# Optimization experiments

Measured on AMD Instinct MI355X. Metric: run time of the kernel, lower is better.

## Reference

```python
import jax, jax.numpy as jnp
import numpy as np

NUM_GROUPS = 32
EPS = 1e-6


def setup_inputs() -> dict:
    key = jax.random.key(0)
    ks = jax.random.split(key, 8)
    B, C, H, W = 2, 512, 64, 64
    s = 1.0 / np.sqrt(C)
    return {
        "x": jax.random.normal(ks[0], (B, C, H, W), dtype=jnp.float32),
        "norm_w": jnp.ones((C,), jnp.float32),
        "norm_b": jnp.zeros((C,), jnp.float32),
        "wq": jax.random.normal(ks[1], (C, C), dtype=jnp.float32) * s,
        "bq": jnp.zeros((C,), jnp.float32),
        "wk": jax.random.normal(ks[2], (C, C), dtype=jnp.float32) * s,
        "bk": jnp.zeros((C,), jnp.float32),
        "wv": jax.random.normal(ks[3], (C, C), dtype=jnp.float32) * s,
        "bv": jnp.zeros((C,), jnp.float32),
        "wp": jax.random.normal(ks[4], (C, C), dtype=jnp.float32) * s,
        "bp": jnp.zeros((C,), jnp.float32),
    }


def _group_norm(x, w, b):
    # x: [B, C, H, W], 32 groups, eps=1e-6, affine
    B, C, H, W = x.shape
    g = x.reshape(B, NUM_GROUPS, C // NUM_GROUPS, H, W)
    mu = jnp.mean(g, axis=(2, 3, 4), keepdims=True)
    var = jnp.mean(jnp.square(g - mu), axis=(2, 3, 4), keepdims=True)
    g = (g - mu) * jax.lax.rsqrt(var + EPS)
    x = g.reshape(B, C, H, W)
    return x * w[None, :, None, None] + b[None, :, None, None]


def _conv1x1(x, w, b):
    # x: [B, C, H, W], w: [out, in] -> [B, out, H, W]
    return jnp.einsum('bchw,oc->bohw', x, w) + b[None, :, None, None]


def reference(x, norm_w, norm_b, wq, bq, wk, bk, wv, bv, wp, bp):
    B, C, H, W = x.shape
    h_ = _group_norm(x, norm_w, norm_b)
    q = _conv1x1(h_, wq, bq)  # [B, C, H, W]
    k = _conv1x1(h_, wk, bk)
    v = _conv1x1(h_, wv, bv)
    N = H * W
    q = q.reshape(B, C, N).transpose(0, 2, 1)  # b (hw) c
    k = k.reshape(B, C, N)                     # b c (hw)
    v = v.reshape(B, C, N)                     # b c (hw)
    scale = jnp.asarray(int(C) ** (-0.5), x.dtype)
    w_ = jnp.einsum('bic,bcj->bij', q, k) * scale   # [B, N, N]
    w_ = jax.nn.softmax(w_, axis=-1)
    # NOTE: no transpose of w_ (faithful to the source): out[:,:,j] = sum_i v[:,:,i] w_[:,i,j]
    h_ = jnp.einsum('bci,bij->bcj', v, w_)          # [B, C, N]
    h_ = h_.reshape(B, C, H, W)
    h_ = _conv1x1(h_, wp, bp)
    return x + h_
```

## Files before the change

kernel.cpp:

```cpp
#include <hip/hip_runtime.h>
#include <hip/hip_bf16.h>

#define BATCH 2
#define CDIM 512
#define NDIM 4096
#define NGROUPS 32
#define CHPG 16
#define GN_EPS 1e-6f

typedef __attribute__((ext_vector_type(8))) short bf16x8;
typedef __attribute__((ext_vector_type(4))) float f32x4;

__device__ __forceinline__ void gl_lds16(const void* g, void* lds) {
  __builtin_amdgcn_global_load_lds((__attribute__((address_space(1))) void*)(g),
                                   (__attribute__((address_space(3))) void*)(lds), 16, 0, 0);
}

template <int N>
__device__ __forceinline__ void wait_vmcnt() {
  if constexpr (N == 2) asm volatile("s_waitcnt vmcnt(2)" ::: "memory");
  else if constexpr (N == 3) asm volatile("s_waitcnt vmcnt(3)" ::: "memory");
  else asm volatile("s_waitcnt vmcnt(4)" ::: "memory");
}

__device__ __forceinline__ void raw_barrier() {
  asm volatile("s_barrier" ::: "memory");
}

__global__ __launch_bounds__(256) void gn_stats_p1(const float* __restrict__ x,
                                                   float2* __restrict__ part) {
  int blk = blockIdx.x;
  int chunk = blk & 15, bg = blk >> 4;
  const float4* p = (const float4*)(x + (size_t)bg * (CHPG * NDIM) + chunk * 4096);
  float s = 0.f, ss = 0.f;
#pragma unroll
  for (int t = 0; t < 4; t++) {
    float4 v = p[threadIdx.x + t * 256];
    s += v.x + v.y + v.z + v.w;
    ss += v.x * v.x + v.y * v.y + v.z * v.z + v.w * v.w;
  }
  int w = threadIdx.x >> 6, l = threadIdx.x & 63;
#pragma unroll
  for (int off = 32; off > 0; off >>= 1) {
    s += __shfl_down(s, off);
    ss += __shfl_down(ss, off);
  }
  __shared__ float r1[4], r2[4];
  if (l == 0) { r1[w] = s; r2[w] = ss; }
  __syncthreads();
  if (threadIdx.x == 0)
    part[blk] = make_float2(r1[0] + r1[1] + r1[2] + r1[3], r2[0] + r2[1] + r2[2] + r2[3]);
}

__global__ __launch_bounds__(64) void gn_stats_p2(const float2* __restrict__ part,
                                                  float2* __restrict__ stats) {
  int bg = threadIdx.x;
  float s = 0.f, ss = 0.f;
#pragma unroll
  for (int c = 0; c < 16; c++) {
    float2 v = part[bg * 16 + c];
    s += v.x; ss += v.y;
  }
  const float inv = 1.0f / (CHPG * NDIM);
  float mean = s * inv;
  float var = ss * inv - mean * mean;
  stats[bg] = make_float2(mean, rsqrtf(var + GN_EPS));
}

__global__ __launch_bounds__(256) void gn_apply_t(const float* __restrict__ x,
                                                  const float2* __restrict__ stats,
                                                  const float* __restrict__ w,
                                                  const float* __restrict__ bias,
                                                  __hip_bfloat16* __restrict__ ht) {
  __shared__ __hip_bfloat16 tile[64][66];
  int b = blockIdx.z, c0 = blockIdx.y * 64, n0 = blockIdx.x * 64;
  int tq = threadIdx.x >> 6;
  int tl = threadIdx.x & 63;
#pragma unroll
  for (int i = 0; i < 16; i++) {
    int cl = tq * 16 + i;
    int c = c0 + cl;
    float2 st = stats[b * NGROUPS + (c >> 4)];
    float v = x[((size_t)b * CDIM + c) * NDIM + n0 + tl];
    v = (v - st.x) * st.y * w[c] + bias[c];
    tile[tl][cl] = __float2bfloat16(v);
  }
  __syncthreads();
#pragma unroll
  for (int i = 0; i < 16; i++) {
    int nl = tq * 16 + i;
    ht[((size_t)b * NDIM + n0 + nl) * CDIM + c0 + tl] = tile[nl][tl];
  }
}

__global__ __launch_bounds__(256) void cvt_w(const float* __restrict__ a, const float* __restrict__ b,
                                             const float* __restrict__ c, const float* __restrict__ d,
                                             __hip_bfloat16* __restrict__ o) {
  int i = blockIdx.x * 256 + threadIdx.x;
  o[i]          = __float2bfloat16(a[i]);
  o[i + 262144] = __float2bfloat16(b[i]);
  o[i + 524288] = __float2bfloat16(c[i]);
  o[i + 786432] = __float2bfloat16(d[i]);
}

template <int MT, int NT, int BIAS_MODE, bool HAS_RES, int OUT_MODE, bool STATS, bool SWIZ, int MINB>
__global__ __launch_bounds__(256, MINB) void mfma_gemm_nt(
    const __hip_bfloat16* __restrict__ A, const __hip_bfloat16* __restrict__ B,
    const float* __restrict__ bias, const float* __restrict__ res,
    void* __restrict__ Cout, float* __restrict__ pmax_g, float* __restrict__ psum_g,
    int M, int N, int K, long sA, long sB, long sC, float scale) {
  constexpr int MTI = MT / 32, NTI = NT / 32;
  constexpr int ABYT = MT * 64;
  constexpr int BBYT = NT * 64;
  constexpr int BUFB = ABYT + BBYT;
  constexpr int NL = (MT == 128 ? 2 : 1) + (NT == 128 ? 2 : 1);
  __shared__ char smem[2 * BUFB];
  const int tid = threadIdx.x;
  const int w = tid >> 6, l = tid & 63;
  const int wy = w >> 1, wx = w & 1;
  const int bz = blockIdx.z;
  int bx = blockIdx.x, by = blockIdx.y;
  if constexpr (SWIZ) {
    int l2 = by * 8 + bx;
    int xcd = l2 & 7, s = l2 >> 3;
    by = xcd + (s & 3) * 8;
    bx = s >> 2;
  }
  const int m0 = by * MT, n0 = bx * NT;
  f32x4 acc[MTI][NTI] = {};
  const int arow = w * (MT / 4) + (l >> 2);
  const int brow = w * (NT / 4) + (l >> 2);
  const char* Ag = (const char*)(A + (size_t)bz * sA + (size_t)(m0 + arow) * K) + (l & 3) * 16;
  const char* Bg = (const char*)(B + (size_t)bz * sB + (size_t)(n0 + brow) * K) + (l & 3) * 16;
  const size_t radv = (size_t)K * 32;
  const int woffA = w * (MT * 16);
  const int woffB = ABYT + w * (NT * 16);

  auto issue = [&](int buf) {
    char* base = smem + buf * BUFB;
    gl_lds16(Ag, base + woffA);
    if (MT == 128) gl_lds16(Ag + radv, base + woffA + 1024);
    gl_lds16(Bg, base + woffB);
    if (NT == 128) gl_lds16(Bg + radv, base + woffB + 1024);
    Ag += 64; Bg += 64;
  };

  issue(0);
  const int T = K / 32;
  for (int t = 0; t < T; t++) {
    issue((t + 1) & 1);
    wait_vmcnt<NL>();
    raw_barrier();
    const __hip_bfloat16* As = (const __hip_bfloat16*)(smem + (t & 1) * BUFB);
    const __hip_bfloat16* Bs = (const __hip_bfloat16*)(smem + (t & 1) * BUFB + ABYT);
    bf16x8 af[MTI], bfr[NTI];
#pragma unroll
    for (int mt = 0; mt < MTI; mt++)
      af[mt] = *(const bf16x8*)(As + (wy * (MT / 2) + mt * 16 + (l & 15)) * 32 + (l >> 4) * 8);
#pragma unroll
    for (int nt = 0; nt < NTI; nt++)
      bfr[nt] = *(const bf16x8*)(Bs + (wx * (NT / 2) + nt * 16 + (l & 15)) * 32 + (l >> 4) * 8);
#pragma unroll
    for (int mt = 0; mt < MTI; mt++)
#pragma unroll
      for (int nt = 0; nt < NTI; nt++)
        acc[mt][nt] = __builtin_amdgcn_mfma_f32_16x16x32_bf16(af[mt], bfr[nt], acc[mt][nt], 0, 0, 0);
    raw_barrier();
  }
  const size_t cbase = (size_t)bz * sC;
#pragma unroll
  for (int mt = 0; mt < MTI; mt++) {
#pragma unroll
    for (int r = 0; r < 4; r++) {
      const int m = m0 + wy * (MT / 2) + mt * 16 + (l >> 4) * 4 + r;
      float bv = (BIAS_MODE == 1) ? bias[m] : 0.f;
#pragma unroll
      for (int nt = 0; nt < NTI; nt++) {
        const int n = n0 + wx * (NT / 2) + nt * 16 + (l & 15);
        float v = acc[mt][nt][r] * scale + bv;
        if (BIAS_MODE == 2) v += bias[n];
        if (HAS_RES) v += res[cbase + (size_t)m * N + n];
        if (OUT_MODE == 0) ((float*)Cout)[cbase + (size_t)m * N + n] = v;
        else ((__hip_bfloat16*)Cout)[cbase + (size_t)m * N + n] = __float2bfloat16(v);
      }
    }
  }
  if constexpr (STATS) {
    float* sred1 = (float*)smem;
    float* sred2 = (float*)smem + 512;
    float cm[NTI];
    __syncthreads();
#pragma unroll
    for (int nt = 0; nt < NTI; nt++) {
      float m = -1e30f;
#pragma unroll
      for (int mt = 0; mt < MTI; mt++)
#pragma unroll
        for (int r = 0; r < 4; r++) m = fmaxf(m, acc[mt][nt][r] * scale);
      m = fmaxf(m, __shfl_xor(m, 16));
      m = fmaxf(m, __shfl_xor(m, 32));
      if (l < 16) sred1[(w * NTI + nt) * 16 + l] = m;
    }
    __syncthreads();
#pragma unroll
    for (int nt = 0; nt < NTI; nt++) {
      float bm = fmaxf(sred1[(wx * NTI + nt) * 16 + (l & 15)],
                       sred1[((2 + wx) * NTI + nt) * 16 + (l & 15)]);
      cm[nt] = bm;
      float s = 0.f;
#pragma unroll
      for (int mt = 0; mt < MTI; mt++)
#pragma unroll
        for (int r = 0; r < 4; r++) s += __expf(acc[mt][nt][r] * scale - bm);
      s += __shfl_xor(s, 16);
      s += __shfl_xor(s, 32);
      if (l < 16) sred2[(w * NTI + nt) * 16 + l] = s;
    }
    __syncthreads();
    if (wy == 0 && l < 16) {
#pragma unroll
      for (int nt = 0; nt < NTI; nt++) {
        float stot = sred2[(wx * NTI + nt) * 16 + l] + sred2[((2 + wx) * NTI + nt) * 16 + l];
        int i = n0 + wx * 64 + nt * 16 + l;
        size_t idx = ((size_t)bz * gridDim.y + blockIdx.y) * N + i;
        pmax_g[idx] = cm[nt];
        psum_g[idx] = stot;
      }
    }
  }
}

__global__ __launch_bounds__(256) void softmax_comb(const float* __restrict__ pmax,
                                                    const float* __restrict__ psum,
                                                    float* __restrict__ cmax, float* __restrict__ cinv) {
  int idx = blockIdx.x * 256 + threadIdx.x;
  int b = idx >> 12, i = idx & (NDIM - 1);
  float M = -1e30f;
  for (int bc = 0; bc < 32; bc++) M = fmaxf(M, pmax[((size_t)b * 32 + bc) * NDIM + i]);
  float s = 0.f;
  for (int bc = 0; bc < 32; bc++) {
    size_t o = ((size_t)b * 32 + bc) * NDIM + i;
    s += psum[o] * __expf(pmax[o] - M);
  }
  cmax[idx] = M;
  cinv[idx] = 1.0f / s;
}

__device__ __forceinline__ short bf16_bits(float v) {
  __hip_bfloat16 h = __float2bfloat16(v);
  union { __hip_bfloat16 h; short s; } u;
  u.h = h;
  return u.s;
}

__global__ __launch_bounds__(256) void softmax_apply(__hip_bfloat16* __restrict__ St,
                                                     const float* __restrict__ cmax,
                                                     const float* __restrict__ cinv) {
  int b = blockIdx.y;
  size_t row = blockIdx.x;
  int i0 = threadIdx.x * 16;
  __hip_bfloat16* p = St + ((size_t)b * NDIM + row) * NDIM + i0;
  const float4* pm = (const float4*)(cmax + (size_t)b * NDIM + i0);
  const float4* pz = (const float4*)(cinv + (size_t)b * NDIM + i0);
  bf16x8 d0 = *(const bf16x8*)p;
  bf16x8 d1 = *(const bf16x8*)(p + 8);
  float4 M4[4], Z4[4];
#pragma unroll
  for (int t = 0; t < 4; t++) { M4[t] = pm[t]; Z4[t] = pz[t]; }
  const float* Mf = (const float*)M4;
  const float* Zf = (const float*)Z4;
  bf16x8 o0, o1;
#pragma unroll
  for (int e = 0; e < 8; e++) {
    union { short s; __hip_bfloat16 h; } u; u.s = d0[e];
    o0[e] = bf16_bits(__expf(__bfloat162float(u.h) - Mf[e]) * Zf[e]);
  }
#pragma unroll
  for (int e = 0; e < 8; e++) {
    union { short s; __hip_bfloat16 h; } u; u.s = d1[e];
    o1[e] = bf16_bits(__expf(__bfloat162float(u.h) - Mf[8 + e]) * Zf[8 + e]);
  }
  *(bf16x8*)p = o0;
  *(bf16x8*)(p + 8) = o1;
}

extern "C" void kernel_launch(void* const* d_in, const int* in_sizes, int n_in,
                              void* d_out, int out_size, void* d_ws, size_t ws_size,
                              hipStream_t stream) {
  const float* x      = (const float*)d_in[0];
  const float* norm_w = (const float*)d_in[1];
  const float* norm_b = (const float*)d_in[2];
  const float* wq = (const float*)d_in[3];
  const float* bq = (const float*)d_in[4];
  const float* wk = (const float*)d_in[5];
  const float* bk = (const float*)d_in[6];
  const float* wv = (const float*)d_in[7];
  const float* bv = (const float*)d_in[8];
  const float* wp = (const float*)d_in[9];
  const float* bp = (const float*)d_in[10];
  float* out = (float*)d_out;

  const long CN = (long)CDIM * NDIM;
  const long NN = (long)NDIM * NDIM;
  char* p = (char*)d_ws;
  auto carve = [&](size_t bytes) { char* r = p; p += (bytes + 255) & ~(size_t)255; return r; };
  __hip_bfloat16* h_t  = (__hip_bfloat16*)carve(BATCH * CN * 2);
  __hip_bfloat16* wb   = (__hip_bfloat16*)carve(4 * 512 * 512 * 2);
  __hip_bfloat16* q_t  = (__hip_bfloat16*)carve(BATCH * CN * 2);
  __hip_bfloat16* k_t  = (__hip_bfloat16*)carve(BATCH * CN * 2);
  __hip_bfloat16* vb   = (__hip_bfloat16*)carve(BATCH * CN * 2);
  __hip_bfloat16* ht2  = (__hip_bfloat16*)carve(BATCH * CN * 2);
  __hip_bfloat16* St   = (__hip_bfloat16*)carve(BATCH * NN * 2);
  float2* stats = (float2*)carve(BATCH * NGROUPS * sizeof(float2));
  float2* gnpart = (float2*)carve(1024 * sizeof(float2));
  float* pmax = (float*)carve((size_t)BATCH * 32 * NDIM * 4);
  float* psum = (float*)carve((size_t)BATCH * 32 * NDIM * 4);
  float* cmax = (float*)carve(BATCH * NDIM * 4);
  float* cinv = (float*)carve(BATCH * NDIM * 4);
  __hip_bfloat16* wbq = wb;
  __hip_bfloat16* wbk = wb + 262144;
  __hip_bfloat16* wbv = wb + 524288;
  __hip_bfloat16* wbp = wb + 786432;

  const float scale = 0.044194173824159216f;

  gn_stats_p1<<<dim3(1024), 256, 0, stream>>>(x, gnpart);
  gn_stats_p2<<<dim3(1), 64, 0, stream>>>(gnpart, stats);
  gn_apply_t<<<dim3(NDIM / 64, CDIM / 64, BATCH), 256, 0, stream>>>(x, stats, norm_w, norm_b, h_t);
  cvt_w<<<dim3(1024), 256, 0, stream>>>(wq, wk, wv, wp, wb);

  mfma_gemm_nt<128, 64, 2, false, 1, false, true, 2><<<dim3(8, 32, BATCH), 256, 0, stream>>>(
      h_t, wbq, bq, nullptr, q_t, nullptr, nullptr, NDIM, CDIM, CDIM, CN, 0, CN, 1.0f);
  mfma_gemm_nt<128, 64, 2, false, 1, false, true, 2><<<dim3(8, 32, BATCH), 256, 0, stream>>>(
      h_t, wbk, bk, nullptr, k_t, nullptr, nullptr, NDIM, CDIM, CDIM, CN, 0, CN, 1.0f);
  mfma_gemm_nt<64, 128, 1, false, 1, false, false, 2><<<dim3(32, 8, BATCH), 256, 0, stream>>>(
      wbv, h_t, bv, nullptr, vb, nullptr, nullptr, CDIM, NDIM, CDIM, 0, CN, CN, 1.0f);
  mfma_gemm_nt<128, 128, 0, false, 1, true, false, 3><<<dim3(32, 32, BATCH), 256, 0, stream>>>(
      k_t, q_t, nullptr, nullptr, St, pmax, psum, NDIM, NDIM, CDIM, CN, CN, NN, scale);
  softmax_comb<<<dim3(32), 256, 0, stream>>>(pmax, psum, cmax, cinv);
  softmax_apply<<<dim3(NDIM, BATCH), 256, 0, stream>>>(St, cmax, cinv);
  mfma_gemm_nt<128, 64, 0, false, 1, false, true, 2><<<dim3(8, 32, BATCH), 256, 0, stream>>>(
      St, vb, nullptr, nullptr, ht2, nullptr, nullptr, NDIM, CDIM, NDIM, NN, CN, CN, 1.0f);
  mfma_gemm_nt<64, 128, 1, true, 0, false, false, 2><<<dim3(32, 8, BATCH), 256, 0, stream>>>(
      wbp, ht2, bp, x, out, nullptr, nullptr, CDIM, NDIM, CDIM, 0, CN, CN, 1.0f);
}
```

Before: 271.4 us.

## Add K-unroll template parameter and XOR-swizzle LDS layout in MFMA GEMM

Adds a KU template parameter so most GEMMs stage a 64-wide K slice per pipeline step instead of 32. This halves the number of barrier and wait iterations. It also rotates the 16-byte chunk offsets when loading global data into LDS and when reading fragments, to avoid LDS bank conflicts on the fragment reads. The cost is larger shared-memory buffers per block and more outstanding loads per stage, which may reduce occupancy. The S=K^T Q GEMM keeps KU=1 but still gets the swizzle.

```diff
diff --git a/kernel.cpp b/kernel.cpp
--- a/kernel.cpp
+++ b/kernel.cpp
@@ -18,9 +18,13 @@
 
 template <int N>
 __device__ __forceinline__ void wait_vmcnt() {
-  if constexpr (N == 2) asm volatile("s_waitcnt vmcnt(2)" ::: "memory");
+  if constexpr (N == 1) asm volatile("s_waitcnt vmcnt(1)" ::: "memory");
+  else if constexpr (N == 2) asm volatile("s_waitcnt vmcnt(2)" ::: "memory");
   else if constexpr (N == 3) asm volatile("s_waitcnt vmcnt(3)" ::: "memory");
-  else asm volatile("s_waitcnt vmcnt(4)" ::: "memory");
+  else if constexpr (N == 4) asm volatile("s_waitcnt vmcnt(4)" ::: "memory");
+  else if constexpr (N == 5) asm volatile("s_waitcnt vmcnt(5)" ::: "memory");
+  else if constexpr (N == 6) asm volatile("s_waitcnt vmcnt(6)" ::: "memory");
+  else asm volatile("s_waitcnt vmcnt(8)" ::: "memory");
 }
 
 __device__ __forceinline__ void raw_barrier() {
@@ -103,17 +107,19 @@
   o[i + 786432] = __float2bfloat16(d[i]);
 }
 
-template <int MT, int NT, int BIAS_MODE, bool HAS_RES, int OUT_MODE, bool STATS, bool SWIZ, int MINB>
+template <int MT, int NT, int KU, int BIAS_MODE, bool HAS_RES, int OUT_MODE, bool STATS, bool SWIZ, int MINB>
 __global__ __launch_bounds__(256, MINB) void mfma_gemm_nt(
     const __hip_bfloat16* __restrict__ A, const __hip_bfloat16* __restrict__ B,
     const float* __restrict__ bias, const float* __restrict__ res,
     void* __restrict__ Cout, float* __restrict__ pmax_g, float* __restrict__ psum_g,
     int M, int N, int K, long sA, long sB, long sC, float scale) {
   constexpr int MTI = MT / 32, NTI = NT / 32;
-  constexpr int ABYT = MT * 64;
-  constexpr int BBYT = NT * 64;
+  constexpr int SB = 64 * KU;
+  constexpr int ABYT = MT * SB, BBYT = NT * SB;
   constexpr int BUFB = ABYT + BBYT;
-  constexpr int NL = (MT == 128 ? 2 : 1) + (NT == 128 ? 2 : 1);
+  constexpr int AISS = MT * KU / 64, BISS = NT * KU / 64;
+  constexpr int NL = AISS + BISS;
+  constexpr int RPI = 16 / KU;
   __shared__ char smem[2 * BUFB];
   const int tid = threadIdx.x;
   const int w = tid >> 6, l = tid & 63;
@@ -128,43 +134,61 @@
   }
   const int m0 = by * MT, n0 = bx * NT;
   f32x4 acc[MTI][NTI] = {};
-  const int arow = w * (MT / 4) + (l >> 2);
-  const int brow = w * (NT / 4) + (l >> 2);
-  const char* Ag = (const char*)(A + (size_t)bz * sA + (size_t)(m0 + arow) * K) + (l & 3) * 16;
-  const char* Bg = (const char*)(B + (size_t)bz * sB + (size_t)(n0 + brow) * K) + (l & 3) * 16;
-  const size_t radv = (size_t)K * 32;
-  const int woffA = w * (MT * 16);
-  const int woffB = ABYT + w * (NT * 16);
+
+  int so;
+  if constexpr (KU == 1) so = (((l & 3) - (l >> 2) - (l >> 4)) & 3) * 16;
+  else                   so = (((l & 7) - (l >> 3)) & 7) * 16;
+  const int lrow = (KU == 1) ? (l >> 2) : (l >> 3);
+  const int arow = w * (MT / 4) + lrow;
+  const int brow = w * (NT / 4) + lrow;
+  const char* Ag = (const char*)A + ((size_t)bz * sA + (size_t)(m0 + arow) * K) * 2 + so;
+  const char* Bg = (const char*)B + ((size_t)bz * sB + (size_t)(n0 + brow) * K) * 2 + so;
+  const size_t iadv = (size_t)RPI * K * 2;
+  const int woffA = w * (MT / 4) * SB;
+  const int woffB = ABYT + w * (NT / 4) * SB;
 
   auto issue = [&](int buf) {
     char* base = smem + buf * BUFB;
-    gl_lds16(Ag, base + woffA);
-    if (MT == 128) gl_lds16(Ag + radv, base + woffA + 1024);
-    gl_lds16(Bg, base + woffB);
-    if (NT == 128) gl_lds16(Bg + radv, base + woffB + 1024);
-    Ag += 64; Bg += 64;
+#pragma unroll
+    for (int i = 0; i < AISS; i++) gl_lds16(Ag + i * iadv, base + woffA + i * 1024);
+#pragma unroll
+    for (int i = 0; i < BISS; i++) gl_lds16(Bg + i * iadv, base + woffB + i * 1024);
+    Ag += SB; Bg += SB;
   };
 
+  const int x = l & 15;
+  int qr0, qr1 = 0;
+  if constexpr (KU == 1) {
+    qr0 = (((l >> 4) + x + (x >> 2)) & 3) * 16;
+  } else {
+    qr0 = (((l >> 4) + (l & 7)) & 7) * 16;
+    qr1 = (((l >> 4) + 4 + (l & 7)) & 7) * 16;
+  }
+
   issue(0);
-  const int T = K / 32;
+  const int T = K / (32 * KU);
   for (int t = 0; t < T; t++) {
     issue((t + 1) & 1);
     wait_vmcnt<NL>();
     raw_barrier();
-    const __hip_bfloat16* As = (const __hip_bfloat16*)(smem + (t & 1) * BUFB);
-    const __hip_bfloat16* Bs = (const __hip_bfloat16*)(smem + (t & 1) * BUFB + ABYT);
-    bf16x8 af[MTI], bfr[NTI];
-#pragma unroll
-    for (int mt = 0; mt < MTI; mt++)
-      af[mt] = *(const bf16x8*)(As + (wy * (MT / 2) + mt * 16 + (l & 15)) * 32 + (l >> 4) * 8);
-#pragma unroll
-    for (int nt = 0; nt < NTI; nt++)
-      bfr[nt] = *(const bf16x8*)(Bs + (wx * (NT / 2) + nt * 16 + (l & 15)) * 32 + (l >> 4) * 8);
-#pragma unroll
-    for (int mt = 0; mt < MTI; mt++)
+    const char* Asb = smem + (t & 1) * BUFB;
+    const char* Bsb = Asb + ABYT;
+#pragma unroll
+    for (int h = 0; h < KU; h++) {
+      const int q = (h == 0) ? qr0 : qr1;
+      bf16x8 af[MTI], bfr[NTI];
+#pragma unroll
+      for (int mt = 0; mt < MTI; mt++)
+        af[mt] = *(const bf16x8*)(Asb + (wy * (MT / 2) + mt * 16 + x) * SB + q);
 #pragma unroll
       for (int nt = 0; nt < NTI; nt++)
-        acc[mt][nt] = __builtin_amdgcn_mfma_f32_16x16x32_bf16(af[mt], bfr[nt], acc[mt][nt], 0, 0, 0);
+        bfr[nt] = *(const bf16x8*)(Bsb + (wx * (NT / 2) + nt * 16 + x) * SB + q);
+#pragma unroll
+      for (int mt = 0; mt < MTI; mt++)
+#pragma unroll
+        for (int nt = 0; nt < NTI; nt++)
+          acc[mt][nt] = __builtin_amdgcn_mfma_f32_16x16x32_bf16(af[mt], bfr[nt], acc[mt][nt], 0, 0, 0);
+    }
     raw_barrier();
   }
   const size_t cbase = (size_t)bz * sC;
@@ -329,18 +353,18 @@
   gn_apply_t<<<dim3(NDIM / 64, CDIM / 64, BATCH), 256, 0, stream>>>(x, stats, norm_w, norm_b, h_t);
   cvt_w<<<dim3(1024), 256, 0, stream>>>(wq, wk, wv, wp, wb);
 
-  mfma_gemm_nt<128, 64, 2, false, 1, false, true, 2><<<dim3(8, 32, BATCH), 256, 0, stream>>>(
+  mfma_gemm_nt<128, 64, 2, 2, false, 1, false, true, 2><<<dim3(8, 32, BATCH), 256, 0, stream>>>(
       h_t, wbq, bq, nullptr, q_t, nullptr, nullptr, NDIM, CDIM, CDIM, CN, 0, CN, 1.0f);
-  mfma_gemm_nt<128, 64, 2, false, 1, false, true, 2><<<dim3(8, 32, BATCH), 256, 0, stream>>>(
+  mfma_gemm_nt<128, 64, 2, 2, false, 1, false, true, 2><<<dim3(8, 32, BATCH), 256, 0, stream>>>(
       h_t, wbk, bk, nullptr, k_t, nullptr, nullptr, NDIM, CDIM, CDIM, CN, 0, CN, 1.0f);
-  mfma_gemm_nt<64, 128, 1, false, 1, false, false, 2><<<dim3(32, 8, BATCH), 256, 0, stream>>>(
+  mfma_gemm_nt<64, 128, 2, 1, false, 1, false, false, 2><<<dim3(32, 8, BATCH), 256, 0, stream>>>(
       wbv, h_t, bv, nullptr, vb, nullptr, nullptr, CDIM, NDIM, CDIM, 0, CN, CN, 1.0f);
-  mfma_gemm_nt<128, 128, 0, false, 1, true, false, 3><<<dim3(32, 32, BATCH), 256, 0, stream>>>(
+  mfma_gemm_nt<128, 128, 1, 0, false, 1, true, false, 3><<<dim3(32, 32, BATCH), 256, 0, stream>>>(
       k_t, q_t, nullptr, nullptr, St, pmax, psum, NDIM, NDIM, CDIM, CN, CN, NN, scale);
   softmax_comb<<<dim3(32), 256, 0, stream>>>(pmax, psum, cmax, cinv);
   softmax_apply<<<dim3(NDIM, BATCH), 256, 0, stream>>>(St, cmax, cinv);
-  mfma_gemm_nt<128, 64, 0, false, 1, false, true, 2><<<dim3(8, 32, BATCH), 256, 0, stream>>>(
+  mfma_gemm_nt<128, 64, 2, 0, false, 1, false, true, 2><<<dim3(8, 32, BATCH), 256, 0, stream>>>(
       St, vb, nullptr, nullptr, ht2, nullptr, nullptr, NDIM, CDIM, NDIM, NN, CN, CN, 1.0f);
-  mfma_gemm_nt<64, 128, 1, true, 0, false, false, 2><<<dim3(32, 8, BATCH), 256, 0, stream>>>(
+  mfma_gemm_nt<64, 128, 2, 1, true, 0, false, false, 2><<<dim3(32, 8, BATCH), 256, 0, stream>>>(
       wbp, ht2, bp, x, out, nullptr, nullptr, CDIM, NDIM, CDIM, 0, CN, CN, 1.0f);
 }
```

Result: faster. 259.8 us (-4.3%).
